# Performance work log

Measured on AMD Instinct MI355X. Metric: run time of the kernel, lower is better.

Reference implementation:

```python
import jax, jax.numpy as jnp
import numpy as np

ITEMS_TOTAL = 50000
DIM = 64
BATCH = 16
N_PER_GRAPH = 50


def setup_inputs() -> dict:
    key = jax.random.key(0)
    k1, k2, k3, k4 = jax.random.split(key, 4)
    nodes = jax.random.randint(k1, (BATCH * N_PER_GRAPH,), 0, ITEMS_TOTAL, dtype=jnp.int64)
    nodes_output = jax.random.normal(k2, (BATCH * N_PER_GRAPH, DIM), dtype=jnp.float32)
    emb_table = jax.random.normal(k3, (ITEMS_TOTAL, DIM), dtype=jnp.float32)
    alpha = jax.random.uniform(k4, (ITEMS_TOTAL, 1), dtype=jnp.float32)  # torch.rand init
    return {"nodes": nodes, "nodes_output": nodes_output, "emb_table": emb_table,
            "alpha": alpha, "n_per_graph": N_PER_GRAPH}


def reference(nodes, nodes_output, emb_table, alpha, n_per_graph):
    items_total, dim = emb_table.shape
    n = int(n_per_graph)
    b = nodes.shape[0] // n
    idx_b = nodes.reshape(b, n)            # (B, n) item indices per graph
    feat_b = nodes_output.reshape(b, n, dim)  # (B, n, F)

    def per_graph(idx, feat):
        # beta: 1 for items present in this graph, 0 otherwise
        beta = jnp.zeros((items_total, 1), dtype=emb_table.dtype).at[idx].set(1.0)
        # gate the full table: untouched rows keep emb, touched rows scaled by (1-alpha)
        embed = (1.0 - beta * alpha) * emb_table          # (items_total, F)
        updated = embed[idx] + alpha[idx] * feat          # (n, F)
        return embed.at[idx].set(updated)

    return jax.vmap(per_graph)(idx_b, feat_b)             # (B, items_total, F)
```

## Files before the change

### kernel.cpp

```cpp
#include <hip/hip_runtime.h>


#define DIM 64
#define SEGS (DIM / 4)
#define BLOCK 256
#define KF 5
#define TILE (BLOCK * KF)
#define NROWS (TILE / SEGS)

__global__ __launch_bounds__(BLOCK) void ggu_stream(
    const int* __restrict__ nodes,
    const float4* __restrict__ feat,
    const float4* __restrict__ emb,
    const float* __restrict__ alpha,
    float4* __restrict__ out,
    int items, int n)
{
    const int b = blockIdx.y;
    const size_t rowsF4 = (size_t)items * SEGS;
    const size_t base   = (size_t)blockIdx.x * TILE;
    const int row0      = (int)(base / SEGS);

    __shared__ int lastj[NROWS];
    for (int i = threadIdx.x; i < NROWS; i += BLOCK) lastj[i] = -1;
    __syncthreads();
    for (int j = threadIdx.x; j < n; j += BLOCK) {
        const int local = nodes[b * n + j] - row0;
        if ((unsigned)local < (unsigned)NROWS)
            atomicMax(&lastj[local], j);
    }
    __syncthreads();

    const float4* e = emb + base;
    float4* o = out + (size_t)b * rowsF4 + base;

    #pragma unroll
    for (int k = 0; k < KF; ++k) {
        const int off = k * BLOCK + (int)threadIdx.x;
        if (base + (size_t)off < rowsF4) {
            float4 v = e[off];
            const int jl = lastj[off >> 4];
            if (jl >= 0) {
                const int row = row0 + (off >> 4);
                const float a = alpha[row];
                const float4 f = feat[(size_t)(b * n + jl) * SEGS + (off & (SEGS - 1))];
                const float om = 1.0f - a;
                v.x = om * v.x + a * f.x;
                v.y = om * v.y + a * f.y;
                v.z = om * v.z + a * f.z;
                v.w = om * v.w + a * f.w;
            }
            o[off] = v;
        }
    }
}

extern "C" void kernel_launch(void* const* d_in, const int* in_sizes, int n_in,
                              void* d_out, int out_size, void* d_ws, size_t ws_size,
                              hipStream_t stream) {
    const int*   nodes = (const int*)d_in[0];
    const float* feat  = (const float*)d_in[1];
    const float* emb   = (const float*)d_in[2];
    const float* alpha = (const float*)d_in[3];

    const int items = in_sizes[3];
    const int B     = out_size / (items * DIM);
    const int n     = in_sizes[0] / B;

    const size_t rowsF4 = (size_t)items * SEGS;
    const unsigned gx = (unsigned)((rowsF4 + TILE - 1) / TILE);
    dim3 grid(gx, (unsigned)B);

    ggu_stream<<<grid, BLOCK, 0, stream>>>(
        nodes, (const float4*)feat, (const float4*)emb, alpha,
        (float4*)d_out, items, n);
}
```

Before: 235.4 us.

## Load each embedding tile once and broadcast it to all batch outputs

The grid is now 1D over table tiles instead of tiles × batch. Each block loads its embedding tile into registers once and writes it to all B output slices, so the table is read once instead of B times. Per-batch last-writer indices are built in dynamic LDS for every graph at once, and a bitmask lets untouched batches skip the update path. In exchange each block does B times more work with fewer blocks, and every block scans all B·n node indices.

```diff
diff --git a/kernel.cpp b/kernel.cpp
--- a/kernel.cpp
+++ b/kernel.cpp
@@ -8,49 +8,76 @@
 #define TILE (BLOCK * KF)
 #define NROWS (TILE / SEGS)
 
-__global__ __launch_bounds__(BLOCK) void ggu_stream(
+template <int CB>
+__global__ __launch_bounds__(BLOCK) void ggu_bcast(
     const int* __restrict__ nodes,
     const float4* __restrict__ feat,
     const float4* __restrict__ emb,
     const float* __restrict__ alpha,
     float4* __restrict__ out,
-    int items, int n)
+    int items, int n, int Brt)
 {
-    const int b = blockIdx.y;
+    const int B = (CB > 0) ? CB : Brt;
     const size_t rowsF4 = (size_t)items * SEGS;
     const size_t base   = (size_t)blockIdx.x * TILE;
     const int row0      = (int)(base / SEGS);
+    const int tid       = threadIdx.x;
 
-    __shared__ int lastj[NROWS];
-    for (int i = threadIdx.x; i < NROWS; i += BLOCK) lastj[i] = -1;
+    extern __shared__ int smem[];
+    int* lastj = smem;
+    unsigned* tmaskp = (unsigned*)(smem + B * NROWS);
+
+    for (int t = tid; t < B * NROWS; t += BLOCK) lastj[t] = -1;
+    if (tid == 0) *tmaskp = 0u;
     __syncthreads();
-    for (int j = threadIdx.x; j < n; j += BLOCK) {
-        const int local = nodes[b * n + j] - row0;
-        if ((unsigned)local < (unsigned)NROWS)
-            atomicMax(&lastj[local], j);
+    const int total = B * n;
+    for (int t = tid; t < total; t += BLOCK) {
+        const int local = nodes[t] - row0;
+        if ((unsigned)local < (unsigned)NROWS) {
+            const int b = t / n;
+            atomicMax(&lastj[b * NROWS + local], t);
+            atomicOr(tmaskp, 1u << b);
+        }
     }
     __syncthreads();
+    const unsigned tm = *tmaskp;
 
+    float4 v[KF];
     const float4* e = emb + base;
-    float4* o = out + (size_t)b * rowsF4 + base;
-
     #pragma unroll
     for (int k = 0; k < KF; ++k) {
-        const int off = k * BLOCK + (int)threadIdx.x;
-        if (base + (size_t)off < rowsF4) {
-            float4 v = e[off];
-            const int jl = lastj[off >> 4];
-            if (jl >= 0) {
-                const int row = row0 + (off >> 4);
-                const float a = alpha[row];
-                const float4 f = feat[(size_t)(b * n + jl) * SEGS + (off & (SEGS - 1))];
-                const float om = 1.0f - a;
-                v.x = om * v.x + a * f.x;
-                v.y = om * v.y + a * f.y;
-                v.z = om * v.z + a * f.z;
-                v.w = om * v.w + a * f.w;
+        const size_t off = (size_t)(k * BLOCK + tid);
+        v[k] = (base + off < rowsF4) ? e[off] : float4{0, 0, 0, 0};
+    }
+
+    for (int b = 0; b < B; ++b) {
+        float4* ob = out + (size_t)b * rowsF4 + base;
+        if (!((tm >> b) & 1u)) {
+            #pragma unroll
+            for (int k = 0; k < KF; ++k) {
+                const size_t off = (size_t)(k * BLOCK + tid);
+                if (base + off < rowsF4) ob[off] = v[k];
             }
-            o[off] = v;
+        } else {
+            #pragma unroll
+            for (int k = 0; k < KF; ++k) {
+                const size_t off = (size_t)(k * BLOCK + tid);
+                if (base + off >= rowsF4) continue;
+                float4 t4 = v[k];
+                const int ioff = k * BLOCK + tid;
+                const int jl = lastj[b * NROWS + (ioff >> 4)];
+                if (jl >= 0) {
+                    const int row = row0 + (ioff >> 4);
+                    const float a = alpha[row];
+                    const float4 f = feat[(size_t)jl * SEGS + (ioff & (SEGS - 1))];
+                    const float om = 1.0f - a;
+                    t4.x = om * t4.x + a * f.x;
+                    t4.y = om * t4.y + a * f.y;
+                    t4.z = om * t4.z + a * f.z;
+                    t4.w = om * t4.w + a * f.w;
+                }
+                ob[off] = t4;
+            }
         }
     }
 }
@@ -68,10 +95,16 @@
     const int n     = in_sizes[0] / B;
 
     const size_t rowsF4 = (size_t)items * SEGS;
-    const unsigned gx = (unsigned)((rowsF4 + TILE - 1) / TILE);
-    dim3 grid(gx, (unsigned)B);
+    const unsigned grid = (unsigned)((rowsF4 + TILE - 1) / TILE);
+    const size_t lds_bytes = (size_t)(B * NROWS + 1) * sizeof(int);
 
-    ggu_stream<<<grid, BLOCK, 0, stream>>>(
-        nodes, (const float4*)feat, (const float4*)emb, alpha,
-        (float4*)d_out, items, n);
+    if (B == 16) {
+        ggu_bcast<16><<<grid, BLOCK, lds_bytes, stream>>>(
+            nodes, (const float4*)feat, (const float4*)emb, alpha,
+            (float4*)d_out, items, n, B);
+    } else {
+        ggu_bcast<0><<<grid, BLOCK, lds_bytes, stream>>>(
+            nodes, (const float4*)feat, (const float4*)emb, alpha,
+            (float4*)d_out, items, n, B);
+    }
 }
```

After: 220.3 us. -6.4%, faster.
